# Performance work log

Measured on AMD Instinct MI355X. Metric: run time of the kernel, lower is better.

Reference implementation:

```python
import jax, jax.numpy as jnp
import numpy as np


def setup_inputs() -> dict:
    key = jax.random.key(0)
    k1, k2, k3, k4 = jax.random.split(key, 4)
    B, C_in, E = 8, 32, 100000
    C_out, K = 64, 5
    x = jax.random.normal(k1, (B, C_in, E, 1), dtype=jnp.float32)
    gemm_edges = jax.random.randint(k2, (B, E, 4), 0, E, dtype=jnp.int32)
    fan_in = C_in * K
    weight = jax.random.normal(k3, (C_out, C_in, 1, K), dtype=jnp.float32) / np.sqrt(fan_in)
    bias = jax.random.normal(k4, (C_out,), dtype=jnp.float32) * 0.01
    return {"x": x, "gemm_edges": gemm_edges, "weight": weight, "bias": bias}


def reference(x, gemm_edges, weight, bias):
    # x: (B, C, E, 1) edge features; gemm_edges: (B, E, 4) ring-neighbor indices
    xs = x[..., 0]                                   # (B, C, E)
    B, C, E = xs.shape
    # prepend self index -> (B, E, 5); +1 shifts into padded table (slot 0 = zero pad)
    idx_self = jnp.broadcast_to(jnp.arange(E, dtype=gemm_edges.dtype)[None, :, None], (B, E, 1))
    Gi = jnp.concatenate([idx_self, gemm_edges], axis=2) + 1  # (B, E, 5)
    xp = jnp.pad(xs, ((0, 0), (0, 0), (1, 0)))       # (B, C, E+1) with zero column at index 0
    # per-batch gather: f[b, c, e, k] = xp[b, c, Gi[b, e, k]]
    f = jnp.take_along_axis(xp, Gi.reshape(B, 1, E * 5), axis=2).reshape(B, C, E, 5)
    f0, f1, f2, f3, f4 = (f[..., i] for i in range(5))
    # symmetric functions for neighbor-order invariance
    G = jnp.stack([f0, f1 + f3, f2 + f4, jnp.abs(f1 - f3), jnp.abs(f2 - f4)], axis=3)  # (B, C, E, 5)
    # Conv2d kernel (1, 5) == contraction over (C, k), output (B, C_out, E, 1)
    out = jnp.einsum('bcek,ock->boe', G, weight[:, :, 0, :]) + bias[None, :, None]
    return out[..., None]
```

## Files before the change

### kernel.cpp

```cpp
#include <hip/hip_runtime.h>
#include <stdint.h>

#define E_TOTAL 100000
#define B_TOTAL 8
#define CIN 32
#define COUT 64
#define TILES 1563
#define NUNITS 782
#define NBLK 256

typedef short bf16x8 __attribute__((ext_vector_type(8)));
typedef float f32x4  __attribute__((ext_vector_type(4)));
typedef int   i32x4  __attribute__((ext_vector_type(4)));
typedef unsigned u32x4 __attribute__((ext_vector_type(4)));

union U16x8 { u32x4 u; bf16x8 s; };

__device__ inline float blo(unsigned u) { return __uint_as_float(u << 16); }
__device__ inline float bhi(unsigned u) { return __uint_as_float(u & 0xffff0000u); }
__device__ inline unsigned bpack(float lo, float hi) {
    return (__float_as_uint(lo) >> 16) | (__float_as_uint(hi) & 0xffff0000u);
}
__device__ inline unsigned badd(unsigned a, unsigned b) {
    return bpack(blo(a) + blo(b), bhi(a) + bhi(b));
}
__device__ inline unsigned babsdiff(unsigned a, unsigned b) {
    return bpack(fabsf(blo(a) - blo(b)), fabsf(bhi(a) - bhi(b)));
}
__device__ inline u32x4 vadd4(u32x4 a, u32x4 b) {
    u32x4 r;
#pragma unroll
    for (int i = 0; i < 4; i++) r[i] = badd(a[i], b[i]);
    return r;
}
__device__ inline u32x4 vabsdiff4(u32x4 a, u32x4 b) {
    u32x4 r;
#pragma unroll
    for (int i = 0; i < 4; i++) r[i] = babsdiff(a[i], b[i]);
    return r;
}
__device__ inline unsigned rne16(float f) {
    unsigned b = __float_as_uint(f);
    b += 0x7fffu + ((b >> 16) & 1u);
    return b >> 16;
}

__global__ __launch_bounds__(256) void prep_transpose(
    const float* __restrict__ x, unsigned* __restrict__ xt,
    const float* __restrict__ w, unsigned short* __restrict__ wb) {
    const int tid = threadIdx.x;
    if (blockIdx.x >= TILES * 8) {
        for (int idx = tid; idx < 4 * 5 * 64 * 8; idx += 256) {
            int j = idx & 7;
            int lane = (idx >> 3) & 63;
            int tg = idx >> 9;
            int g = tg % 5;
            int t = tg / 5;
            int nn = lane & 15, qq = lane >> 4;
            int o = nn + 16 * t;
            int c = qq * 8 + j;
            wb[idx] = (unsigned short)rne16(w[(o * CIN + c) * 5 + g]);
        }
        return;
    }
    __shared__ float tbuf[CIN][65];
    const int b = blockIdx.x & 7;
    const int e0 = (blockIdx.x >> 3) * 64;
    const int el = tid & 63;
    const int cw = tid >> 6;
#pragma unroll
    for (int i = 0; i < 8; i++) {
        int c = cw * 8 + i;
        int e = e0 + el;
        float v = (e < E_TOTAL)
            ? __builtin_nontemporal_load(x + ((size_t)b * CIN + c) * E_TOTAL + e)
            : 0.f;
        tbuf[c][el] = v;
    }
    __syncthreads();
    const int c2 = tid & 15;
#pragma unroll
    for (int i = 0; i < 4; i++) {
        int el2 = (tid >> 4) * 4 + i;
        int e = e0 + el2;
        if (e < E_TOTAL) {
            unsigned lo = rne16(tbuf[c2 * 2][el2]);
            unsigned hi = rne16(tbuf[c2 * 2 + 1][el2]);
            xt[((size_t)b * E_TOTAL + e) * 16 + c2] = lo | (hi << 16);
        }
    }
}

__global__ __launch_bounds__(256) void meshconv_main(
    const unsigned short* __restrict__ xt,
    const int* __restrict__ ge,
    const u32x4* __restrict__ wb,
    const float* __restrict__ bias,
    float* __restrict__ out) {
    __shared__ u32x4 wlds[1280];
    const int tid = threadIdx.x;
    const int lane = tid & 63;
    const int wv = tid >> 6;
    const int b = blockIdx.x & 7;
    const int blk = blockIdx.x >> 3;
    const int n = lane & 15;
    const int q = lane >> 4;
    const int co = q * 8;

#pragma unroll
    for (int k = 0; k < 5; k++) wlds[tid + k * 256] = wb[tid + k * 256];
    __syncthreads();

    const unsigned short* xb = xt + (size_t)b * E_TOTAL * CIN;
    const int* geb = ge + (size_t)b * E_TOTAL * 4;
    float bv[4];
#pragma unroll
    for (int t = 0; t < 4; t++) bv[t] = bias[n + 16 * t];

    int u = blk;
    int e0 = u * 128 + wv * 32;
    bool act = (u < NUNITS) && (e0 < E_TOTAL);
    i32x4 nid0, nid1;
    u32x4 s0, s1;
    if (act) {
        nid0 = __builtin_nontemporal_load((const i32x4*)(geb + (size_t)(e0 + n) * 4));
        nid1 = __builtin_nontemporal_load((const i32x4*)(geb + (size_t)(e0 + 16 + n) * 4));
        s0 = *(const u32x4*)(xb + (size_t)(e0 + n) * CIN + co);
        s1 = *(const u32x4*)(xb + (size_t)(e0 + 16 + n) * CIN + co);
    }

    for (; u < NUNITS; u += NBLK) {
        const int un = u + NBLK;
        const int e0n = un * 128 + wv * 32;
        const bool actn = (un < NUNITS) && (e0n < E_TOTAL);

        u32x4 g10, g20, g30, g40, g11, g21, g31, g41;
        if (act) {
            g10 = *(const u32x4*)(xb + (size_t)nid0[0] * CIN + co);
            g20 = *(const u32x4*)(xb + (size_t)nid0[1] * CIN + co);
            g30 = *(const u32x4*)(xb + (size_t)nid0[2] * CIN + co);
            g40 = *(const u32x4*)(xb + (size_t)nid0[3] * CIN + co);
            g11 = *(const u32x4*)(xb + (size_t)nid1[0] * CIN + co);
            g21 = *(const u32x4*)(xb + (size_t)nid1[1] * CIN + co);
            g31 = *(const u32x4*)(xb + (size_t)nid1[2] * CIN + co);
            g41 = *(const u32x4*)(xb + (size_t)nid1[3] * CIN + co);
        }
        i32x4 nid0n, nid1n;
        u32x4 s0n, s1n;
        if (actn) {
            nid0n = __builtin_nontemporal_load((const i32x4*)(geb + (size_t)(e0n + n) * 4));
            nid1n = __builtin_nontemporal_load((const i32x4*)(geb + (size_t)(e0n + 16 + n) * 4));
            s0n = *(const u32x4*)(xb + (size_t)(e0n + n) * CIN + co);
            s1n = *(const u32x4*)(xb + (size_t)(e0n + 16 + n) * CIN + co);
        }

        if (act) {
            u32x4 A0[5], A1[5];
            A0[0] = s0;
            A0[1] = vadd4(g10, g30);
            A0[2] = vadd4(g20, g40);
            A0[3] = vabsdiff4(g10, g30);
            A0[4] = vabsdiff4(g20, g40);
            A1[0] = s1;
            A1[1] = vadd4(g11, g31);
            A1[2] = vadd4(g21, g41);
            A1[3] = vabsdiff4(g11, g31);
            A1[4] = vabsdiff4(g21, g41);

            f32x4 acc0[4], acc1[4];
#pragma unroll
            for (int t = 0; t < 4; t++)
#pragma unroll
                for (int r = 0; r < 4; r++) { acc0[t][r] = 0.f; acc1[t][r] = 0.f; }

#pragma unroll
            for (int g = 0; g < 5; g++) {
                U16x8 av0; av0.u = A0[g];
                U16x8 av1; av1.u = A1[g];
#pragma unroll
                for (int t = 0; t < 4; t++) {
                    U16x8 bw; bw.u = wlds[(t * 5 + g) * 64 + lane];
                    acc0[t] = __builtin_amdgcn_mfma_f32_16x16x32_bf16(av0.s, bw.s, acc0[t], 0, 0, 0);
                    acc1[t] = __builtin_amdgcn_mfma_f32_16x16x32_bf16(av1.s, bw.s, acc1[t], 0, 0, 0);
                }
            }

#pragma unroll
            for (int t = 0; t < 4; t++) {
                const int o = n + 16 * t;
                float* orow = out + ((size_t)b * COUT + o) * E_TOTAL + e0 + q * 4;
                f32x4 r0 = acc0[t] + bv[t];
                f32x4 r1 = acc1[t] + bv[t];
                __builtin_nontemporal_store(r0, (f32x4*)orow);
                __builtin_nontemporal_store(r1, (f32x4*)(orow + 16));
            }
        }

        nid0 = nid0n; nid1 = nid1n; s0 = s0n; s1 = s1n;
        e0 = e0n; act = actn;
    }
}

__global__ __launch_bounds__(256) void meshconv_fallback(
    const float* __restrict__ x, const int* __restrict__ ge,
    const float* __restrict__ w, const float* __restrict__ bias,
    float* __restrict__ out) {
    __shared__ float f[5][32];
    __shared__ float G[5][32];
    __shared__ int idxs[4];
    const int e = blockIdx.x, b = blockIdx.y;
    const int tid = threadIdx.x;
    if (tid < 4) idxs[tid] = ge[((size_t)b * E_TOTAL + e) * 4 + tid];
    __syncthreads();
    if (tid < 160) {
        int k = tid >> 5, c = tid & 31;
        int src = (k == 0) ? e : idxs[k - 1];
        f[k][c] = x[((size_t)b * CIN + c) * E_TOTAL + src];
    }
    __syncthreads();
    if (tid < 32) {
        int c = tid;
        G[0][c] = f[0][c];
        G[1][c] = f[1][c] + f[3][c];
        G[2][c] = f[2][c] + f[4][c];
        G[3][c] = fabsf(f[1][c] - f[3][c]);
        G[4][c] = fabsf(f[2][c] - f[4][c]);
    }
    __syncthreads();
    if (tid < COUT) {
        float acc = bias[tid];
        for (int c = 0; c < CIN; c++)
#pragma unroll
            for (int g = 0; g < 5; g++)
                acc += G[g][c] * w[(tid * CIN + c) * 5 + g];
        out[((size_t)b * COUT + tid) * E_TOTAL + e] = acc;
    }
}

extern "C" void kernel_launch(void* const* d_in, const int* in_sizes, int n_in,
                              void* d_out, int out_size, void* d_ws, size_t ws_size,
                              hipStream_t stream) {
    const float* x = (const float*)d_in[0];
    const int* ge = (const int*)d_in[1];
    const float* w = (const float*)d_in[2];
    const float* bias = (const float*)d_in[3];
    float* out = (float*)d_out;

    const size_t xt_bytes = (size_t)B_TOTAL * E_TOTAL * CIN * 2;
    const size_t need = 65536 + xt_bytes;
    if (ws_size < need) {
        dim3 grid(E_TOTAL, B_TOTAL);
        meshconv_fallback<<<grid, 256, 0, stream>>>(x, ge, w, bias, out);
        return;
    }
    unsigned short* wb = (unsigned short*)d_ws;
    unsigned short* xt = (unsigned short*)((char*)d_ws + 65536);

    prep_transpose<<<TILES * 8 + 1, 256, 0, stream>>>(x, (unsigned*)xt, w, wb);
    meshconv_main<<<NBLK * 8, 256, 0, stream>>>(xt, ge, (const u32x4*)wb, bias, out);
}
```

Before: 374.1 us.

## Switch to fp16 packed math and deepen gather prefetch pipeline by one stage

Replaces the bf16 storage and emulated bf16 add/absdiff (unpack to fp32, repack) with fp16, using native packed half vector add/sub plus a sign mask, and switches the MFMA to the f16 variant. The main loop is restructured into a two-stage software pipeline: neighbor-row gathers for the next unit are issued before the current unit's MFMAs, and index/self loads run two units ahead. Bias is folded into the accumulator initialisation. The aim is to cut VALU work and hide gather latency, at the cost of more live registers and fp16 range/precision in place of bf16.

```diff
diff --git a/kernel.cpp b/kernel.cpp
--- a/kernel.cpp
+++ b/kernel.cpp
@@ -9,40 +9,23 @@
 #define NUNITS 782
 #define NBLK 256
 
-typedef short bf16x8 __attribute__((ext_vector_type(8)));
 typedef float f32x4  __attribute__((ext_vector_type(4)));
 typedef int   i32x4  __attribute__((ext_vector_type(4)));
 typedef unsigned u32x4 __attribute__((ext_vector_type(4)));
-
-union U16x8 { u32x4 u; bf16x8 s; };
-
-__device__ inline float blo(unsigned u) { return __uint_as_float(u << 16); }
-__device__ inline float bhi(unsigned u) { return __uint_as_float(u & 0xffff0000u); }
-__device__ inline unsigned bpack(float lo, float hi) {
-    return (__float_as_uint(lo) >> 16) | (__float_as_uint(hi) & 0xffff0000u);
-}
-__device__ inline unsigned badd(unsigned a, unsigned b) {
-    return bpack(blo(a) + blo(b), bhi(a) + bhi(b));
-}
-__device__ inline unsigned babsdiff(unsigned a, unsigned b) {
-    return bpack(fabsf(blo(a) - blo(b)), fabsf(bhi(a) - bhi(b)));
-}
-__device__ inline u32x4 vadd4(u32x4 a, u32x4 b) {
-    u32x4 r;
-#pragma unroll
-    for (int i = 0; i < 4; i++) r[i] = badd(a[i], b[i]);
-    return r;
-}
-__device__ inline u32x4 vabsdiff4(u32x4 a, u32x4 b) {
-    u32x4 r;
-#pragma unroll
-    for (int i = 0; i < 4; i++) r[i] = babsdiff(a[i], b[i]);
-    return r;
-}
-__device__ inline unsigned rne16(float f) {
-    unsigned b = __float_as_uint(f);
-    b += 0x7fffu + ((b >> 16) & 1u);
-    return b >> 16;
+typedef _Float16 h16x8 __attribute__((ext_vector_type(8)));
+
+union HU { u32x4 u; h16x8 h; };
+
+__device__ inline unsigned pkh(float lo, float hi) {
+    auto r = __builtin_amdgcn_cvt_pkrtz(lo, hi);
+    return __builtin_bit_cast(unsigned, r);
+}
+__device__ inline h16x8 ash(u32x4 v) { HU x; x.u = v; return x.h; }
+__device__ inline h16x8 habsd(h16x8 a, h16x8 b) {
+    HU x; x.h = a - b;
+#pragma unroll
+    for (int i = 0; i < 4; i++) x.u[i] &= 0x7fff7fffu;
+    return x.h;
 }
 
 __global__ __launch_bounds__(256) void prep_transpose(
@@ -59,7 +42,8 @@
             int nn = lane & 15, qq = lane >> 4;
             int o = nn + 16 * t;
             int c = qq * 8 + j;
-            wb[idx] = (unsigned short)rne16(w[(o * CIN + c) * 5 + g]);
+            _Float16 hv = (_Float16)w[(o * CIN + c) * 5 + g];
+            wb[idx] = __builtin_bit_cast(unsigned short, hv);
         }
         return;
     }
@@ -84,9 +68,8 @@
         int el2 = (tid >> 4) * 4 + i;
         int e = e0 + el2;
         if (e < E_TOTAL) {
-            unsigned lo = rne16(tbuf[c2 * 2][el2]);
-            unsigned hi = rne16(tbuf[c2 * 2 + 1][el2]);
-            xt[((size_t)b * E_TOTAL + e) * 16 + c2] = lo | (hi << 16);
+            xt[((size_t)b * E_TOTAL + e) * 16 + c2] =
+                pkh(tbuf[c2 * 2][el2], tbuf[c2 * 2 + 1][el2]);
         }
     }
 }
@@ -120,84 +103,104 @@
     int u = blk;
     int e0 = u * 128 + wv * 32;
     bool act = (u < NUNITS) && (e0 < E_TOTAL);
-    i32x4 nid0, nid1;
-    u32x4 s0, s1;
+    i32x4 nidA0, nidA1;
+    u32x4 sA0, sA1;
     if (act) {
-        nid0 = __builtin_nontemporal_load((const i32x4*)(geb + (size_t)(e0 + n) * 4));
-        nid1 = __builtin_nontemporal_load((const i32x4*)(geb + (size_t)(e0 + 16 + n) * 4));
-        s0 = *(const u32x4*)(xb + (size_t)(e0 + n) * CIN + co);
-        s1 = *(const u32x4*)(xb + (size_t)(e0 + 16 + n) * CIN + co);
+        nidA0 = __builtin_nontemporal_load((const i32x4*)(geb + (size_t)(e0 + n) * 4));
+        nidA1 = __builtin_nontemporal_load((const i32x4*)(geb + (size_t)(e0 + 16 + n) * 4));
+        sA0 = *(const u32x4*)(xb + (size_t)(e0 + n) * CIN + co);
+        sA1 = *(const u32x4*)(xb + (size_t)(e0 + 16 + n) * CIN + co);
+    }
+    u32x4 g10, g20, g30, g40, g11, g21, g31, g41;
+    if (act) {
+        g10 = *(const u32x4*)(xb + (size_t)nidA0[0] * CIN + co);
+        g20 = *(const u32x4*)(xb + (size_t)nidA0[1] * CIN + co);
+        g30 = *(const u32x4*)(xb + (size_t)nidA0[2] * CIN + co);
+        g40 = *(const u32x4*)(xb + (size_t)nidA0[3] * CIN + co);
+        g11 = *(const u32x4*)(xb + (size_t)nidA1[0] * CIN + co);
+        g21 = *(const u32x4*)(xb + (size_t)nidA1[1] * CIN + co);
+        g31 = *(const u32x4*)(xb + (size_t)nidA1[2] * CIN + co);
+        g41 = *(const u32x4*)(xb + (size_t)nidA1[3] * CIN + co);
+    }
+    int un = u + NBLK;
+    int e0n = un * 128 + wv * 32;
+    bool actn = (un < NUNITS) && (e0n < E_TOTAL);
+    i32x4 nidB0, nidB1;
+    u32x4 sB0, sB1;
+    if (actn) {
+        nidB0 = __builtin_nontemporal_load((const i32x4*)(geb + (size_t)(e0n + n) * 4));
+        nidB1 = __builtin_nontemporal_load((const i32x4*)(geb + (size_t)(e0n + 16 + n) * 4));
+        sB0 = *(const u32x4*)(xb + (size_t)(e0n + n) * CIN + co);
+        sB1 = *(const u32x4*)(xb + (size_t)(e0n + 16 + n) * CIN + co);
     }
 
     for (; u < NUNITS; u += NBLK) {
-        const int un = u + NBLK;
-        const int e0n = un * 128 + wv * 32;
-        const bool actn = (un < NUNITS) && (e0n < E_TOTAL);
-
-        u32x4 g10, g20, g30, g40, g11, g21, g31, g41;
+        const int e0c = u * 128 + wv * 32;
+
+        h16x8 A0[5], A1[5];
         if (act) {
-            g10 = *(const u32x4*)(xb + (size_t)nid0[0] * CIN + co);
-            g20 = *(const u32x4*)(xb + (size_t)nid0[1] * CIN + co);
-            g30 = *(const u32x4*)(xb + (size_t)nid0[2] * CIN + co);
-            g40 = *(const u32x4*)(xb + (size_t)nid0[3] * CIN + co);
-            g11 = *(const u32x4*)(xb + (size_t)nid1[0] * CIN + co);
-            g21 = *(const u32x4*)(xb + (size_t)nid1[1] * CIN + co);
-            g31 = *(const u32x4*)(xb + (size_t)nid1[2] * CIN + co);
-            g41 = *(const u32x4*)(xb + (size_t)nid1[3] * CIN + co);
-        }
-        i32x4 nid0n, nid1n;
-        u32x4 s0n, s1n;
+            A0[0] = ash(sA0);
+            A0[1] = ash(g10) + ash(g30);
+            A0[2] = ash(g20) + ash(g40);
+            A0[3] = habsd(ash(g10), ash(g30));
+            A0[4] = habsd(ash(g20), ash(g40));
+            A1[0] = ash(sA1);
+            A1[1] = ash(g11) + ash(g31);
+            A1[2] = ash(g21) + ash(g41);
+            A1[3] = habsd(ash(g11), ash(g31));
+            A1[4] = habsd(ash(g21), ash(g41));
+        }
+
         if (actn) {
-            nid0n = __builtin_nontemporal_load((const i32x4*)(geb + (size_t)(e0n + n) * 4));
-            nid1n = __builtin_nontemporal_load((const i32x4*)(geb + (size_t)(e0n + 16 + n) * 4));
-            s0n = *(const u32x4*)(xb + (size_t)(e0n + n) * CIN + co);
-            s1n = *(const u32x4*)(xb + (size_t)(e0n + 16 + n) * CIN + co);
+            g10 = *(const u32x4*)(xb + (size_t)nidB0[0] * CIN + co);
+            g20 = *(const u32x4*)(xb + (size_t)nidB0[1] * CIN + co);
+            g30 = *(const u32x4*)(xb + (size_t)nidB0[2] * CIN + co);
+            g40 = *(const u32x4*)(xb + (size_t)nidB0[3] * CIN + co);
+            g11 = *(const u32x4*)(xb + (size_t)nidB1[0] * CIN + co);
+            g21 = *(const u32x4*)(xb + (size_t)nidB1[1] * CIN + co);
+            g31 = *(const u32x4*)(xb + (size_t)nidB1[2] * CIN + co);
+            g41 = *(const u32x4*)(xb + (size_t)nidB1[3] * CIN + co);
+        }
+
+        u32x4 sN0 = sB0, sN1 = sB1;
+        const int u2 = u + 2 * NBLK;
+        const int e02 = u2 * 128 + wv * 32;
+        const bool act2 = (u2 < NUNITS) && (e02 < E_TOTAL);
+        if (act2) {
+            nidB0 = __builtin_nontemporal_load((const i32x4*)(geb + (size_t)(e02 + n) * 4));
+            nidB1 = __builtin_nontemporal_load((const i32x4*)(geb + (size_t)(e02 + 16 + n) * 4));
+            sB0 = *(const u32x4*)(xb + (size_t)(e02 + n) * CIN + co);
+            sB1 = *(const u32x4*)(xb + (size_t)(e02 + 16 + n) * CIN + co);
         }
 
         if (act) {
-            u32x4 A0[5], A1[5];
-            A0[0] = s0;
-            A0[1] = vadd4(g10, g30);
-            A0[2] = vadd4(g20, g40);
-            A0[3] = vabsdiff4(g10, g30);
-            A0[4] = vabsdiff4(g20, g40);
-            A1[0] = s1;
-            A1[1] = vadd4(g11, g31);
-            A1[2] = vadd4(g21, g41);
-            A1[3] = vabsdiff4(g11, g31);
-            A1[4] = vabsdiff4(g21, g41);
-
             f32x4 acc0[4], acc1[4];
 #pragma unroll
             for (int t = 0; t < 4; t++)
 #pragma unroll
-                for (int r = 0; r < 4; r++) { acc0[t][r] = 0.f; acc1[t][r] = 0.f; }
+                for (int r = 0; r < 4; r++) { acc0[t][r] = bv[t]; acc1[t][r] = bv[t]; }
 
 #pragma unroll
             for (int g = 0; g < 5; g++) {
-                U16x8 av0; av0.u = A0[g];
-                U16x8 av1; av1.u = A1[g];
 #pragma unroll
                 for (int t = 0; t < 4; t++) {
-                    U16x8 bw; bw.u = wlds[(t * 5 + g) * 64 + lane];
-                    acc0[t] = __builtin_amdgcn_mfma_f32_16x16x32_bf16(av0.s, bw.s, acc0[t], 0, 0, 0);
-                    acc1[t] = __builtin_amdgcn_mfma_f32_16x16x32_bf16(av1.s, bw.s, acc1[t], 0, 0, 0);
+                    HU bw; bw.u = wlds[(t * 5 + g) * 64 + lane];
+                    acc0[t] = __builtin_amdgcn_mfma_f32_16x16x32_f16(A0[g], bw.h, acc0[t], 0, 0, 0);
+                    acc1[t] = __builtin_amdgcn_mfma_f32_16x16x32_f16(A1[g], bw.h, acc1[t], 0, 0, 0);
                 }
             }
 
 #pragma unroll
             for (int t = 0; t < 4; t++) {
                 const int o = n + 16 * t;
-                float* orow = out + ((size_t)b * COUT + o) * E_TOTAL + e0 + q * 4;
-                f32x4 r0 = acc0[t] + bv[t];
-                f32x4 r1 = acc1[t] + bv[t];
-                __builtin_nontemporal_store(r0, (f32x4*)orow);
-                __builtin_nontemporal_store(r1, (f32x4*)(orow + 16));
+                float* orow = out + ((size_t)b * COUT + o) * E_TOTAL + e0c + q * 4;
+                __builtin_nontemporal_store(acc0[t], (f32x4*)orow);
+                __builtin_nontemporal_store(acc1[t], (f32x4*)(orow + 16));
             }
         }
 
-        nid0 = nid0n; nid1 = nid1n; s0 = s0n; s1 = s1n;
-        e0 = e0n; act = actn;
+        sA0 = sN0; sA1 = sN1;
+        act = actn; actn = act2;
     }
 }
 
```

Measured after the change: 386.2 us. +3.2%, slower.
